# Performance work log

Measured on AMD Instinct MI355X. Metric: run time of the kernel, lower is better.

## Reference

```python
import jax, jax.numpy as jnp
import numpy as np

KH, KW = 3, 3  # window_size[1], window_size[2]
SH, SW = 1, 1  # strides
FILTERS = 64


def _extract_patches(x, kh, kw, sh, sw):
    # TF tf.image.extract_patches ordering: depth = (row, col, channel), channel fastest.
    B, H, W, C = x.shape
    Ho = (H - kh) // sh + 1
    Wo = (W - kw) // sw + 1
    # stack kh*kw shifted views -> (B, Ho, Wo, kh*kw, C)
    views = [x[:, i:i + (Ho - 1) * sh + 1:sh, j:j + (Wo - 1) * sw + 1:sw, :]
             for i in range(kh) for j in range(kw)]
    patches = jnp.stack(views, axis=3)
    return patches.reshape(B, Ho, Wo, kh * kw * C)


def setup_inputs() -> dict:
    key = jax.random.key(0)
    k1, k2 = jax.random.split(key)
    B, H, W, C = 8, 32, 32, 32
    K = KH * KW * C  # 288
    x = jax.random.normal(k1, (B, H, W, C), dtype=jnp.float32)
    w = jax.random.normal(k2, (1, 1, 1, K, FILTERS), dtype=jnp.float32) * 0.05
    bias = jnp.zeros((FILTERS,), dtype=jnp.float32)
    return {"x": x, "w": w, "bias": bias}


def reference(x, w, bias):
    # patches: (B, Ho, Wo, K)
    patches = _extract_patches(x, KH, KW, SH, SW)
    # broadcast add: (B, Ho, Wo, K, F)
    s = patches[..., None] + w
    # tropical max-plus minus min-plus over the patch axis, plus bias
    return jnp.max(s, axis=3) - jnp.min(s, axis=3) + bias
```

## Files before the change

kernel.cpp:

```cpp
#include <hip/hip_runtime.h>
#include <math.h>


#define TPB 512
#define PIX 2
#define NTA 5
#define NTB 4

__device__ __forceinline__ float fmax3(float a, float b, float c) {
    return fmaxf(fmaxf(a, b), c);
}
__device__ __forceinline__ float fmin3(float a, float b, float c) {
    return fminf(fminf(a, b), c);
}

template <int T0, int NT>
__device__ __forceinline__ void compute_taps(
    const float* __restrict__ wl, const float* const* xp, int lane,
    float* amax, float* amin)
{
#pragma unroll
    for (int t = 0; t < NT; ++t) {
        const int tap = T0 + t;
        const int dy = tap / 3;
        const int dx = tap % 3;
        const int xoff = (dy * 32 + dx) * 32;
#pragma unroll
        for (int c = 0; c < 32; c += 4) {
            const float w0 = wl[t * 2048 + (c + 0) * 64 + lane];
            const float w1 = wl[t * 2048 + (c + 1) * 64 + lane];
            const float w2 = wl[t * 2048 + (c + 2) * 64 + lane];
            const float w3 = wl[t * 2048 + (c + 3) * 64 + lane];
#pragma unroll
            for (int p = 0; p < PIX; ++p) {
                const float4 xv = *(const float4*)(xp[p] + xoff + c);
                const float s0 = xv.x + w0;
                const float s1 = xv.y + w1;
                const float s2 = xv.z + w2;
                const float s3 = xv.w + w3;
                amax[p] = fmax3(amax[p], fmax3(s0, s1, s2), s3);
                amin[p] = fmin3(amin[p], fmin3(s0, s1, s2), s3);
            }
        }
    }
}

__global__ __launch_bounds__(TPB) void trop_kernel(
    const float* __restrict__ x,
    const float* __restrict__ w,
    const float* __restrict__ bias,
    float* __restrict__ out)
{
    __shared__ float wlds[NTA * 2048];

    const int tid  = threadIdx.x;
    const int lane = tid & 63;
    const int wv   = tid >> 6;

    const int pix0 = blockIdx.x * (8 * PIX) + wv * PIX;

    const float* xp[PIX];
#pragma unroll
    for (int p = 0; p < PIX; ++p) {
        const int pid = pix0 + p;
        const int wo = pid % 30;
        const int t  = pid / 30;
        const int ho = t % 30;
        const int b  = t / 30;
        xp[p] = x + (((b * 32 + ho) * 32) + wo) * 32;
    }

    {
        const float4* src = (const float4*)w;
        float4* dst = (float4*)wlds;
#pragma unroll
        for (int i = 0; i < 5; ++i) dst[tid + i * 512] = src[tid + i * 512];
    }
    float4 rB[4];
    {
        const float4* src = (const float4*)(w + NTA * 2048);
#pragma unroll
        for (int i = 0; i < 4; ++i) rB[i] = src[tid + i * 512];
    }
    __syncthreads();

    float amax[PIX], amin[PIX];
#pragma unroll
    for (int p = 0; p < PIX; ++p) { amax[p] = -INFINITY; amin[p] = INFINITY; }

    compute_taps<0, NTA>(wlds, xp, lane, amax, amin);

    __syncthreads();
    {
        float4* dst = (float4*)wlds;
#pragma unroll
        for (int i = 0; i < 4; ++i) dst[tid + i * 512] = rB[i];
    }
    __syncthreads();

    compute_taps<NTA, NTB>(wlds, xp, lane, amax, amin);

    const float bv = bias[lane];
#pragma unroll
    for (int p = 0; p < PIX; ++p)
        out[(pix0 + p) * 64 + lane] = amax[p] - amin[p] + bv;
}

extern "C" void kernel_launch(void* const* d_in, const int* in_sizes, int n_in,
                              void* d_out, int out_size, void* d_ws, size_t ws_size,
                              hipStream_t stream) {
    const float* x    = (const float*)d_in[0];
    const float* w    = (const float*)d_in[1];
    const float* bias = (const float*)d_in[2];
    float* out = (float*)d_out;

    trop_kernel<<<dim3(450), dim3(TPB), 0, stream>>>(x, w, bias, out);
}
```

Baseline: 81.42 us.

## Stage all nine weight taps in dynamic LDS and use wave-uniform scalar x offsets

Copies the full 9x2048 weight tensor (72 KB) into dynamic shared memory in one pass. This removes the two-phase staging that held four taps in registers and needed an extra pair of barriers. Pixel base offsets are forced wave-uniform with readfirstlane, so x loads can go through scalar loads instead of per-lane vector float4 loads. The cost is much larger LDS per block, which may limit occupancy, and a one-time host attribute call to allow the bigger allocation.

```diff
diff --git a/kernel.cpp b/kernel.cpp
--- a/kernel.cpp
+++ b/kernel.cpp
@@ -4,8 +4,6 @@
 
 #define TPB 512
 #define PIX 2
-#define NTA 5
-#define NTB 4
 
 __device__ __forceinline__ float fmax3(float a, float b, float c) {
     return fmaxf(fmaxf(a, b), c);
@@ -14,44 +12,13 @@
     return fminf(fminf(a, b), c);
 }
 
-template <int T0, int NT>
-__device__ __forceinline__ void compute_taps(
-    const float* __restrict__ wl, const float* const* xp, int lane,
-    float* amax, float* amin)
-{
-#pragma unroll
-    for (int t = 0; t < NT; ++t) {
-        const int tap = T0 + t;
-        const int dy = tap / 3;
-        const int dx = tap % 3;
-        const int xoff = (dy * 32 + dx) * 32;
-#pragma unroll
-        for (int c = 0; c < 32; c += 4) {
-            const float w0 = wl[t * 2048 + (c + 0) * 64 + lane];
-            const float w1 = wl[t * 2048 + (c + 1) * 64 + lane];
-            const float w2 = wl[t * 2048 + (c + 2) * 64 + lane];
-            const float w3 = wl[t * 2048 + (c + 3) * 64 + lane];
-#pragma unroll
-            for (int p = 0; p < PIX; ++p) {
-                const float4 xv = *(const float4*)(xp[p] + xoff + c);
-                const float s0 = xv.x + w0;
-                const float s1 = xv.y + w1;
-                const float s2 = xv.z + w2;
-                const float s3 = xv.w + w3;
-                amax[p] = fmax3(amax[p], fmax3(s0, s1, s2), s3);
-                amin[p] = fmin3(amin[p], fmin3(s0, s1, s2), s3);
-            }
-        }
-    }
-}
-
 __global__ __launch_bounds__(TPB) void trop_kernel(
     const float* __restrict__ x,
     const float* __restrict__ w,
     const float* __restrict__ bias,
     float* __restrict__ out)
 {
-    __shared__ float wlds[NTA * 2048];
+    extern __shared__ float wlds[];
 
     const int tid  = threadIdx.x;
     const int lane = tid & 63;
@@ -59,7 +26,14 @@
 
     const int pix0 = blockIdx.x * (8 * PIX) + wv * PIX;
 
-    const float* xp[PIX];
+    {
+        const float4* src = (const float4*)w;
+        float4* dst = (float4*)wlds;
+#pragma unroll
+        for (int i = 0; i < 9; ++i) dst[tid + i * 512] = src[tid + i * 512];
+    }
+
+    int xoffp[PIX];
 #pragma unroll
     for (int p = 0; p < PIX; ++p) {
         const int pid = pix0 + p;
@@ -67,38 +41,39 @@
         const int t  = pid / 30;
         const int ho = t % 30;
         const int b  = t / 30;
-        xp[p] = x + (((b * 32 + ho) * 32) + wo) * 32;
+        xoffp[p] = __builtin_amdgcn_readfirstlane((((b * 32 + ho) * 32) + wo) * 32);
     }
-
-    {
-        const float4* src = (const float4*)w;
-        float4* dst = (float4*)wlds;
-#pragma unroll
-        for (int i = 0; i < 5; ++i) dst[tid + i * 512] = src[tid + i * 512];
-    }
-    float4 rB[4];
-    {
-        const float4* src = (const float4*)(w + NTA * 2048);
-#pragma unroll
-        for (int i = 0; i < 4; ++i) rB[i] = src[tid + i * 512];
-    }
-    __syncthreads();
 
     float amax[PIX], amin[PIX];
 #pragma unroll
     for (int p = 0; p < PIX; ++p) { amax[p] = -INFINITY; amin[p] = INFINITY; }
 
-    compute_taps<0, NTA>(wlds, xp, lane, amax, amin);
-
-    __syncthreads();
-    {
-        float4* dst = (float4*)wlds;
-#pragma unroll
-        for (int i = 0; i < 4; ++i) dst[tid + i * 512] = rB[i];
-    }
     __syncthreads();
 
-    compute_taps<NTA, NTB>(wlds, xp, lane, amax, amin);
+#pragma unroll
+    for (int tap = 0; tap < 9; ++tap) {
+        const int dy = tap / 3;
+        const int dx = tap % 3;
+        const int xoff = (dy * 32 + dx) * 32;
+        const float* wl = wlds + tap * 2048;
+#pragma unroll
+        for (int c = 0; c < 32; c += 4) {
+            const float w0 = wl[(c + 0) * 64 + lane];
+            const float w1 = wl[(c + 1) * 64 + lane];
+            const float w2 = wl[(c + 2) * 64 + lane];
+            const float w3 = wl[(c + 3) * 64 + lane];
+#pragma unroll
+            for (int p = 0; p < PIX; ++p) {
+                const float* xb = x + xoffp[p] + xoff;
+                const float s0 = xb[c + 0] + w0;
+                const float s1 = xb[c + 1] + w1;
+                const float s2 = xb[c + 2] + w2;
+                const float s3 = xb[c + 3] + w3;
+                amax[p] = fmax3(amax[p], fmax3(s0, s1, s2), s3);
+                amin[p] = fmin3(amin[p], fmin3(s0, s1, s2), s3);
+            }
+        }
+    }
 
     const float bv = bias[lane];
 #pragma unroll
@@ -114,5 +89,13 @@
     const float* bias = (const float*)d_in[2];
     float* out = (float*)d_out;
 
-    trop_kernel<<<dim3(450), dim3(TPB), 0, stream>>>(x, w, bias, out);
+    static int attr_done = 0;
+    if (!attr_done) {
+        (void)hipFuncSetAttribute((const void*)trop_kernel,
+                                  hipFuncAttributeMaxDynamicSharedMemorySize,
+                                  73728);
+        attr_done = 1;
+    }
+
+    trop_kernel<<<dim3(450), dim3(TPB), 73728, stream>>>(x, w, bias, out);
 }
```

New measurement: 68.04 us, median of 2. 1.2x faster.
